# Kernel optimization log

Measured on AMD Instinct MI355X. Metric: run time of the kernel, lower is better.

## Reference

```python
import jax, jax.numpy as jnp
import numpy as np

D_IN = 1024
D_OUT = 1024
NUM_HEADS = 16
HEAD_DIM = D_OUT // NUM_HEADS


def setup_inputs() -> dict:
    key = jax.random.key(0)
    k_x, k_q, k_k, k_v, k_o = jax.random.split(key, 5)
    # Xavier-uniform-ish init for weights (stored as [d_in, d_out] for x @ W)
    lim = float(np.sqrt(6.0 / (D_IN + D_OUT)) / np.sqrt(2.0))
    lim_o = float(np.sqrt(6.0 / (D_OUT + D_OUT)))
    return {
        "x": jax.random.normal(k_x, (2, 2048, D_IN), dtype=jnp.float32),
        "W_query": jax.random.uniform(k_q, (D_IN, D_OUT), jnp.float32, -lim, lim),
        "W_key": jax.random.uniform(k_k, (D_IN, D_OUT), jnp.float32, -lim, lim),
        "W_value": jax.random.uniform(k_v, (D_IN, D_OUT), jnp.float32, -lim, lim),
        "W_out": jax.random.uniform(k_o, (D_OUT, D_OUT), jnp.float32, -lim_o, lim_o),
        "b_out": jnp.zeros((D_OUT,), dtype=jnp.float32),
    }


def reference(x, W_query, W_key, W_value, W_out, b_out):
    B, S, _ = x.shape
    scale = 1.0 / np.sqrt(HEAD_DIM)

    def split_heads(t):  # [B,S,D] -> [B,H,S,hd]
        return t.reshape(B, S, NUM_HEADS, HEAD_DIM).transpose(0, 2, 1, 3)

    q = split_heads(x @ W_query)
    k = split_heads(x @ W_key)
    v = split_heads(x @ W_value)

    scores = jnp.einsum("bhqd,bhkd->bhqk", q, k) * scale  # [B,H,S,S]
    causal = jnp.tril(jnp.ones((S, S), dtype=bool))  # True = keep
    scores = jnp.where(causal, scores, -jnp.inf)
    weights = jax.nn.softmax(scores, axis=-1)
    ctx = jnp.einsum("bhqk,bhkd->bhqd", weights, v)
    ctx = ctx.transpose(0, 2, 1, 3).reshape(B, S, D_OUT)
    return ctx @ W_out + b_out
```

## Files before the change

kernel.cpp:

```cpp
#include <hip/hip_runtime.h>
#include <hip/hip_bf16.h>


typedef __bf16 bf16_t;
typedef __bf16 bf16x4 __attribute__((ext_vector_type(4)));
typedef __bf16 bf16x8 __attribute__((ext_vector_type(8)));
typedef float f32x4 __attribute__((ext_vector_type(4)));

#define AS_GLOBAL __attribute__((address_space(1)))
#define AS_LDS    __attribute__((address_space(3)))

__device__ __forceinline__ void async_load16(const void* g, void* l) {
    __builtin_amdgcn_global_load_lds((AS_GLOBAL void*)(g), (AS_LDS void*)(l), 16, 0, 0);
}

__device__ __forceinline__ void barrier_lgkm() {
    asm volatile("s_waitcnt lgkmcnt(0)\n\ts_barrier" ::: "memory");
}

__global__ __launch_bounds__(256) void cvt_f32_bf16(const float* __restrict__ src,
                                                    bf16_t* __restrict__ dst, int n4) {
    int i = blockIdx.x * 256 + threadIdx.x;
    if (i < n4) {
        float4 v = ((const float4*)src)[i];
        bf16x4 o;
        o[0] = (bf16_t)v.x; o[1] = (bf16_t)v.y; o[2] = (bf16_t)v.z; o[3] = (bf16_t)v.w;
        ((bf16x4*)dst)[i] = o;
    }
}

__global__ __launch_bounds__(256) void transpose_cvt4(
    const float* __restrict__ W0, const float* __restrict__ W1,
    const float* __restrict__ W2, const float* __restrict__ W3,
    bf16_t* __restrict__ outbase) {
    __shared__ bf16_t T[64][65];
    int t = threadIdx.x;
    int k0 = blockIdx.x * 64, n0 = blockIdx.y * 64, z = blockIdx.z;
    const float* W = (z == 0) ? W0 : (z == 1) ? W1 : (z == 2) ? W2 : W3;
    bf16_t* WT = outbase + (size_t)z * 1048576;
#pragma unroll
    for (int c = 0; c < 4; c++) {
        int idx = c * 256 + t;
        int row = idx >> 4;
        int col4 = (idx & 15) * 4;
        float4 v = *(const float4*)(W + (k0 + row) * 1024 + n0 + col4);
        T[row][col4 + 0] = (bf16_t)v.x;
        T[row][col4 + 1] = (bf16_t)v.y;
        T[row][col4 + 2] = (bf16_t)v.z;
        T[row][col4 + 3] = (bf16_t)v.w;
    }
    __syncthreads();
#pragma unroll
    for (int c = 0; c < 4; c++) {
        int idx = c * 256 + t;
        int nrow = idx >> 4;
        int kc4 = (idx & 15) * 4;
        bf16x4 o;
        o[0] = T[kc4 + 0][nrow];
        o[1] = T[kc4 + 1][nrow];
        o[2] = T[kc4 + 2][nrow];
        o[3] = T[kc4 + 3][nrow];
        *(bf16x4*)(WT + (n0 + nrow) * 1024 + k0 + kc4) = o;
    }
}

__global__ __launch_bounds__(256) void qkv_gemm(
    const bf16_t* __restrict__ A,
    const bf16_t* __restrict__ WqT, const bf16_t* __restrict__ WkT,
    const bf16_t* __restrict__ WvT,
    bf16_t* __restrict__ Qo, bf16_t* __restrict__ Ko, bf16_t* __restrict__ Vo) {
    const int KD = 1024;
    __shared__ __align__(16) bf16_t As[2][4096];
    __shared__ __align__(16) bf16_t Bs[2][4096];
    int tid = threadIdx.x;
    int wave = tid >> 6, lane = tid & 63;
    int quad = lane >> 4, l16 = lane & 15;
    int wm = wave >> 1, wn = wave & 1;
    int z = blockIdx.z;
    const bf16_t* BT = (z == 0) ? WqT : (z == 1) ? WkT : WvT;
    int m0 = blockIdx.x * 128;
    int n0 = blockIdx.y * 128;

    int r = tid >> 2;
    int c8 = (((tid & 3) ^ ((tid >> 3) & 3))) * 8;
    const bf16_t* gA0 = A + (size_t)(m0 + r) * KD + c8;
    const bf16_t* gA1 = A + (size_t)(m0 + 64 + r) * KD + c8;
    const bf16_t* gB0 = BT + (size_t)(n0 + r) * KD + c8;
    const bf16_t* gB1 = BT + (size_t)(n0 + 64 + r) * KD + c8;

    f32x4 acc[4][4];
#pragma unroll
    for (int i = 0; i < 4; i++)
#pragma unroll
        for (int j = 0; j < 4; j++) acc[i][j] = (f32x4){0.f, 0.f, 0.f, 0.f};

    int4 sa0 = *(const int4*)gA0, sa1 = *(const int4*)gA1;
    int4 sb0 = *(const int4*)gB0, sb1 = *(const int4*)gB1;
    *(int4*)(As[0] + tid * 8) = sa0;
    *(int4*)(As[0] + 2048 + tid * 8) = sa1;
    *(int4*)(Bs[0] + tid * 8) = sb0;
    *(int4*)(Bs[0] + 2048 + tid * 8) = sb1;
    sa0 = *(const int4*)(gA0 + 32); sa1 = *(const int4*)(gA1 + 32);
    sb0 = *(const int4*)(gB0 + 32); sb1 = *(const int4*)(gB1 + 32);

    int csw = (quad ^ ((l16 >> 1) & 3)) * 8;
#pragma unroll 1
    for (int kk = 0; kk < 32; kk += 2) {
        barrier_lgkm();
        bf16x8 af[4], bfr[4];
#pragma unroll
        for (int mt = 0; mt < 4; mt++)
            af[mt] = *(const bf16x8*)(As[0] + (wm * 64 + mt * 16 + l16) * 32 + csw);
#pragma unroll
        for (int nt = 0; nt < 4; nt++)
            bfr[nt] = *(const bf16x8*)(Bs[0] + (wn * 64 + nt * 16 + l16) * 32 + csw);
        *(int4*)(As[1] + tid * 8) = sa0;
        *(int4*)(As[1] + 2048 + tid * 8) = sa1;
        *(int4*)(Bs[1] + tid * 8) = sb0;
        *(int4*)(Bs[1] + 2048 + tid * 8) = sb1;
        if (kk + 2 < 32) {
            int k0 = (kk + 2) * 32;
            sa0 = *(const int4*)(gA0 + k0); sa1 = *(const int4*)(gA1 + k0);
            sb0 = *(const int4*)(gB0 + k0); sb1 = *(const int4*)(gB1 + k0);
        }
        if (z == 2) {
#pragma unroll
            for (int mt = 0; mt < 4; mt++)
#pragma unroll
                for (int nt = 0; nt < 4; nt++)
                    acc[mt][nt] = __builtin_amdgcn_mfma_f32_16x16x32_bf16(
                        bfr[nt], af[mt], acc[mt][nt], 0, 0, 0);
        } else {
#pragma unroll
            for (int mt = 0; mt < 4; mt++)
#pragma unroll
                for (int nt = 0; nt < 4; nt++)
                    acc[mt][nt] = __builtin_amdgcn_mfma_f32_16x16x32_bf16(
                        af[mt], bfr[nt], acc[mt][nt], 0, 0, 0);
        }
        barrier_lgkm();
#pragma unroll
        for (int mt = 0; mt < 4; mt++)
            af[mt] = *(const bf16x8*)(As[1] + (wm * 64 + mt * 16 + l16) * 32 + csw);
#pragma unroll
        for (int nt = 0; nt < 4; nt++)
            bfr[nt] = *(const bf16x8*)(Bs[1] + (wn * 64 + nt * 16 + l16) * 32 + csw);
        if (kk + 2 < 32) {
            *(int4*)(As[0] + tid * 8) = sa0;
            *(int4*)(As[0] + 2048 + tid * 8) = sa1;
            *(int4*)(Bs[0] + tid * 8) = sb0;
            *(int4*)(Bs[0] + 2048 + tid * 8) = sb1;
            if (kk + 3 < 32) {
                int k0 = (kk + 3) * 32;
                sa0 = *(const int4*)(gA0 + k0); sa1 = *(const int4*)(gA1 + k0);
                sb0 = *(const int4*)(gB0 + k0); sb1 = *(const int4*)(gB1 + k0);
            }
        }
        if (z == 2) {
#pragma unroll
            for (int mt = 0; mt < 4; mt++)
#pragma unroll
                for (int nt = 0; nt < 4; nt++)
                    acc[mt][nt] = __builtin_amdgcn_mfma_f32_16x16x32_bf16(
                        bfr[nt], af[mt], acc[mt][nt], 0, 0, 0);
        } else {
#pragma unroll
            for (int mt = 0; mt < 4; mt++)
#pragma unroll
                for (int nt = 0; nt < 4; nt++)
                    acc[mt][nt] = __builtin_amdgcn_mfma_f32_16x16x32_bf16(
                        af[mt], bfr[nt], acc[mt][nt], 0, 0, 0);
        }
    }

    if (z == 0) {
#pragma unroll
        for (int mt = 0; mt < 4; mt++) {
            int mg_base = m0 + wm * 64 + mt * 16 + quad * 4;
#pragma unroll
            for (int nt = 0; nt < 4; nt++) {
                int ng = n0 + wn * 64 + nt * 16 + l16;
                int h = ng >> 6, d = ng & 63;
#pragma unroll
                for (int rr = 0; rr < 4; rr++) {
                    int mg = mg_base + rr;
                    int b = mg >> 11, s = mg & 2047;
                    Qo[(((size_t)(b * 16 + h) * 2048) + s) * 64 + d] =
                        (bf16_t)acc[mt][nt][rr];
                }
            }
        }
    } else if (z == 1) {
#pragma unroll
        for (int mt = 0; mt < 4; mt++) {
            int mg_base = m0 + wm * 64 + mt * 16 + quad * 4;
#pragma unroll
            for (int nt = 0; nt < 4; nt++) {
                int ng = n0 + wn * 64 + nt * 16 + l16;
                int h = ng >> 6, dd = ng & 63;
#pragma unroll
                for (int rr = 0; rr < 4; rr++) {
                    int mg = mg_base + rr;
                    int b = mg >> 11, sl = mg & 2047;
                    int kt = sl >> 6, row = sl & 63;
                    int cc = (dd >> 3) ^ (row & 7);
                    Ko[(size_t)(b * 16 + h) * 131072 + kt * 4096 + row * 64 +
                       cc * 8 + (dd & 7)] = (bf16_t)acc[mt][nt][rr];
                }
            }
        }
    } else {
#pragma unroll
        for (int mt = 0; mt < 4; mt++) {
            int sg = m0 + wm * 64 + mt * 16 + l16;
            int b = sg >> 11, sl = sg & 2047;
            int kt = sl >> 6, srow = sl & 63;
#pragma unroll
            for (int nt = 0; nt < 4; nt++) {
                int dg_base = n0 + wn * 64 + nt * 16 + quad * 4;
#pragma unroll
                for (int rr = 0; rr < 4; rr++) {
                    int dg = dg_base + rr;
                    int h = dg >> 6, dd = dg & 63;
                    int cc = (srow >> 3) ^ (dd & 7);
                    Vo[(size_t)(b * 16 + h) * 131072 + kt * 4096 + dd * 64 +
                       cc * 8 + (srow & 7)] = (bf16_t)acc[mt][nt][rr];
                }
            }
        }
    }
}

__device__ __forceinline__ float exp_pwrite(f32x4 sc[4], bf16_t* Ps,
                                            int wave, int quad, int l16) {
    float part = 0.f;
    int rowbase = (wave * 16 + l16) * 64;
    int gran = (quad & 1) * 4;
    int chi = quad >> 1;
#pragma unroll
    for (int nt = 0; nt < 4; nt++) {
        f32x4 p;
#pragma unroll
        for (int rr = 0; rr < 4; rr++) {
            p[rr] = __builtin_amdgcn_exp2f(sc[nt][rr]);
            part += p[rr];
        }
        bf16x4 pb;
#pragma unroll
        for (int rr = 0; rr < 4; rr++) pb[rr] = (bf16_t)p[rr];
        int cc = (nt * 2 + chi) ^ (l16 & 7);
        *(bf16x4*)(Ps + rowbase + cc * 8 + gran) = pb;
    }
    part += __shfl_xor(part, 16);
    part += __shfl_xor(part, 32);
    return part;
}

__global__ __launch_bounds__(256) void attn(
    const bf16_t* __restrict__ Q, const bf16_t* __restrict__ Kt,
    const bf16_t* __restrict__ Vt, bf16_t* __restrict__ ctx) {
    const int S = 2048;
    __shared__ bf16_t Ks[2][4096];
    __shared__ bf16_t Vs[2][4096];
    __shared__ bf16_t Ps[4096];
    int tid = threadIdx.x, wave = tid >> 6, lane = tid & 63;
    int quad = lane >> 4, l16 = lane & 15;

    int f = blockIdx.x + 32 * blockIdx.y;
    int g = f >> 8, s = f & 255;
    int qt = (g & 1) ? (31 - (s & 31)) : (s & 31);
    int bh = (s >> 5) + 8 * g;
    int h = bh & 15, b = bh >> 4;

    const bf16_t* Qbh = Q + (size_t)bh * S * 64;
    const bf16_t* Kbh = Kt + (size_t)bh * 131072;
    const bf16_t* Vbh = Vt + (size_t)bh * 131072;

    const float qs = 0.125f * 1.44269504f;
    bf16x8 aQ[2];
    {
        const bf16_t* rq = Qbh + (size_t)(qt * 64 + wave * 16 + l16) * 64;
#pragma unroll
        for (int ks = 0; ks < 2; ks++) {
            bf16x8 t = *(const bf16x8*)(rq + ks * 32 + quad * 8);
#pragma unroll
            for (int j = 0; j < 8; j++) t[j] = (bf16_t)((float)t[j] * qs);
            aQ[ks] = t;
        }
    }

    float L = 0.f;
    f32x4 O[4];
#pragma unroll
    for (int i = 0; i < 4; i++) O[i] = (f32x4){0.f, 0.f, 0.f, 0.f};

    {
        const bf16_t* kg = Kbh + tid * 8;
        const bf16_t* vg = Vbh + tid * 8;
        async_load16(kg, Ks[0] + wave * 512);
        async_load16(kg + 2048, Ks[0] + 2048 + wave * 512);
        async_load16(vg, Vs[0] + wave * 512);
        async_load16(vg + 2048, Vs[0] + 2048 + wave * 512);
    }
    __syncthreads();

    for (int kt = 0; kt <= qt; kt++) {
        int cur = kt & 1;
        if (kt < qt) {
            const bf16_t* kg = Kbh + (kt + 1) * 4096 + tid * 8;
            const bf16_t* vg = Vbh + (kt + 1) * 4096 + tid * 8;
            async_load16(kg, Ks[cur ^ 1] + wave * 512);
            async_load16(kg + 2048, Ks[cur ^ 1] + 2048 + wave * 512);
            async_load16(vg, Vs[cur ^ 1] + wave * 512);
            async_load16(vg + 2048, Vs[cur ^ 1] + 2048 + wave * 512);
        }

        bf16x8 kf[4][2], vf[4][2];
#pragma unroll
        for (int nt = 0; nt < 4; nt++) {
            const bf16_t* krow = Ks[cur] + (nt * 16 + l16) * 64;
            const bf16_t* vrow = Vs[cur] + (nt * 16 + l16) * 64;
#pragma unroll
            for (int ks = 0; ks < 2; ks++) {
                int csw = ((ks * 4 + quad) ^ (l16 & 7)) * 8;
                kf[nt][ks] = *(const bf16x8*)(krow + csw);
                vf[nt][ks] = *(const bf16x8*)(vrow + csw);
            }
        }

        f32x4 sc[4];
#pragma unroll
        for (int nt = 0; nt < 4; nt++) {
            f32x4 ss = (f32x4){0.f, 0.f, 0.f, 0.f};
            ss = __builtin_amdgcn_mfma_f32_16x16x32_bf16(kf[nt][0], aQ[0], ss, 0, 0, 0);
            ss = __builtin_amdgcn_mfma_f32_16x16x32_bf16(kf[nt][1], aQ[1], ss, 0, 0, 0);
            sc[nt] = ss;
        }
        if (kt == qt) {
            int qg = qt * 64 + wave * 16 + l16;
#pragma unroll
            for (int nt = 0; nt < 4; nt++)
#pragma unroll
                for (int rr = 0; rr < 4; rr++)
                    if (kt * 64 + nt * 16 + quad * 4 + rr > qg) sc[nt][rr] = -1e30f;
        }
        L += exp_pwrite(sc, Ps, wave, quad, l16);

#pragma unroll
        for (int ks = 0; ks < 2; ks++) {
            int csw = ((ks * 4 + quad) ^ (l16 & 7)) * 8;
            bf16x8 aP = *(const bf16x8*)(Ps + (wave * 16 + l16) * 64 + csw);
#pragma unroll
            for (int nt = 0; nt < 4; nt++)
                O[nt] = __builtin_amdgcn_mfma_f32_16x16x32_bf16(aP, vf[nt][ks],
                                                                O[nt], 0, 0, 0);
        }
        __syncthreads();
    }

    float il[4];
#pragma unroll
    for (int rr = 0; rr < 4; rr++) il[rr] = 1.f / __shfl(L, quad * 4 + rr);
#pragma unroll
    for (int nt = 0; nt < 4; nt++) {
#pragma unroll
        for (int rr = 0; rr < 4; rr++) {
            int qoff = wave * 16 + quad * 4 + rr;
            int col = h * 64 + nt * 16 + l16;
            ctx[(size_t)(b * 2048 + qt * 64 + qoff) * 1024 + col] =
                (bf16_t)(O[nt][rr] * il[rr]);
        }
    }
}

__global__ __launch_bounds__(256) void out_gemm(
    const bf16_t* __restrict__ A, const bf16_t* __restrict__ BT,
    const float* __restrict__ bias, float* __restrict__ Cout) {
    const int KD = 1024;
    __shared__ __align__(16) bf16_t As[2][2048];
    __shared__ __align__(16) bf16_t Bs[2][4096];
    int tid = threadIdx.x;
    int wave = tid >> 6, lane = tid & 63;
    int quad = lane >> 4, l16 = lane & 15;
    int wm = wave >> 1, wn = wave & 1;
    int m0 = blockIdx.x * 64;
    int n0 = blockIdx.y * 128;

    int r = tid >> 2;
    int c8 = (((tid & 3) ^ ((tid >> 3) & 3))) * 8;
    const bf16_t* gA  = A + (size_t)(m0 + r) * KD + c8;
    const bf16_t* gB0 = BT + (size_t)(n0 + r) * KD + c8;
    const bf16_t* gB1 = BT + (size_t)(n0 + 64 + r) * KD + c8;

    f32x4 acc[2][4];
#pragma unroll
    for (int i = 0; i < 2; i++)
#pragma unroll
        for (int j = 0; j < 4; j++) acc[i][j] = (f32x4){0.f, 0.f, 0.f, 0.f};

    int4 sa = *(const int4*)gA;
    int4 sb0 = *(const int4*)gB0, sb1 = *(const int4*)gB1;
    *(int4*)(As[0] + tid * 8) = sa;
    *(int4*)(Bs[0] + tid * 8) = sb0;
    *(int4*)(Bs[0] + 2048 + tid * 8) = sb1;
    sa = *(const int4*)(gA + 32);
    sb0 = *(const int4*)(gB0 + 32); sb1 = *(const int4*)(gB1 + 32);

    int csw = (quad ^ ((l16 >> 1) & 3)) * 8;
#pragma unroll 1
    for (int kk = 0; kk < 32; kk += 2) {
        barrier_lgkm();
        bf16x8 af[2], bfr[4];
#pragma unroll
        for (int mt = 0; mt < 2; mt++)
            af[mt] = *(const bf16x8*)(As[0] + (wm * 32 + mt * 16 + l16) * 32 + csw);
#pragma unroll
        for (int nt = 0; nt < 4; nt++)
            bfr[nt] = *(const bf16x8*)(Bs[0] + (wn * 64 + nt * 16 + l16) * 32 + csw);
        *(int4*)(As[1] + tid * 8) = sa;
        *(int4*)(Bs[1] + tid * 8) = sb0;
        *(int4*)(Bs[1] + 2048 + tid * 8) = sb1;
        if (kk + 2 < 32) {
            int k0 = (kk + 2) * 32;
            sa = *(const int4*)(gA + k0);
            sb0 = *(const int4*)(gB0 + k0); sb1 = *(const int4*)(gB1 + k0);
        }
#pragma unroll
        for (int mt = 0; mt < 2; mt++)
#pragma unroll
            for (int nt = 0; nt < 4; nt++)
                acc[mt][nt] = __builtin_amdgcn_mfma_f32_16x16x32_bf16(af[mt], bfr[nt],
                                                                      acc[mt][nt], 0, 0, 0);
        barrier_lgkm();
#pragma unroll
        for (int mt = 0; mt < 2; mt++)
            af[mt] = *(const bf16x8*)(As[1] + (wm * 32 + mt * 16 + l16) * 32 + csw);
#pragma unroll
        for (int nt = 0; nt < 4; nt++)
            bfr[nt] = *(const bf16x8*)(Bs[1] + (wn * 64 + nt * 16 + l16) * 32 + csw);
        if (kk + 2 < 32) {
            *(int4*)(As[0] + tid * 8) = sa;
            *(int4*)(Bs[0] + tid * 8) = sb0;
            *(int4*)(Bs[0] + 2048 + tid * 8) = sb1;
            if (kk + 3 < 32) {
                int k0 = (kk + 3) * 32;
                sa = *(const int4*)(gA + k0);
                sb0 = *(const int4*)(gB0 + k0); sb1 = *(const int4*)(gB1 + k0);
            }
        }
#pragma unroll
        for (int mt = 0; mt < 2; mt++)
#pragma unroll
            for (int nt = 0; nt < 4; nt++)
                acc[mt][nt] = __builtin_amdgcn_mfma_f32_16x16x32_bf16(af[mt], bfr[nt],
                                                                      acc[mt][nt], 0, 0, 0);
    }

#pragma unroll
    for (int mt = 0; mt < 2; mt++) {
        int mg_base = m0 + wm * 32 + mt * 16 + quad * 4;
#pragma unroll
        for (int nt = 0; nt < 4; nt++) {
            int ng = n0 + wn * 64 + nt * 16 + l16;
            float bv = bias[ng];
#pragma unroll
            for (int rr = 0; rr < 4; rr++) {
                int mg = mg_base + rr;
                Cout[(size_t)mg * 1024 + ng] = acc[mt][nt][rr] + bv;
            }
        }
    }
}

extern "C" void kernel_launch(void* const* d_in, const int* in_sizes, int n_in,
                              void* d_out, int out_size, void* d_ws, size_t ws_size,
                              hipStream_t stream) {
    const float* x  = (const float*)d_in[0];
    const float* Wq = (const float*)d_in[1];
    const float* Wk = (const float*)d_in[2];
    const float* Wv = (const float*)d_in[3];
    const float* Wo = (const float*)d_in[4];
    const float* bo = (const float*)d_in[5];
    float* out = (float*)d_out;
    char* ws = (char*)d_ws;

    bf16_t* xb   = (bf16_t*)(ws);
    bf16_t* WTs  = (bf16_t*)(ws + (8u << 20));
    bf16_t* WqT  = WTs;
    bf16_t* WkT  = WTs + 1048576;
    bf16_t* WvT  = WTs + 2097152;
    bf16_t* WoT  = WTs + 3145728;
    bf16_t* Qb   = (bf16_t*)(ws + (16u << 20));
    bf16_t* Kb   = (bf16_t*)(ws + (24u << 20));
    bf16_t* Vb   = (bf16_t*)(ws + (32u << 20));
    bf16_t* ctxb = (bf16_t*)(ws + (40u << 20));

    cvt_f32_bf16<<<4096, 256, 0, stream>>>(x, xb, (4096 * 1024) / 4);
    transpose_cvt4<<<dim3(16, 16, 4), 256, 0, stream>>>(Wq, Wk, Wv, Wo, WTs);
    qkv_gemm<<<dim3(32, 8, 3), 256, 0, stream>>>(xb, WqT, WkT, WvT, Qb, Kb, Vb);
    attn<<<dim3(32, 32), 256, 0, stream>>>(Qb, Kb, Vb, ctxb);
    out_gemm<<<dim3(64, 8), 256, 0, stream>>>(ctxb, WoT, bo, out);
}
```

Baseline: 186.6 us.

## Fuse x conversion into QKV GEMM and process two query tiles per attention block

Removes the separate f32-to-bf16 conversion kernel by loading fp32 x directly in the QKV GEMM and converting to bf16 as tiles are staged into LDS. The attention kernel now handles 128 query rows per block as two 64-row subtiles that share each loaded K/V tile, halving K/V traffic and block count. It also swaps the async global_load_lds path for register-staged prefetch two tiles ahead. Costs include doubled fp32 A-tile global reads in the GEMM, more registers per attention thread, and coarser causal load balance.

```diff
diff --git a/kernel.cpp b/kernel.cpp
--- a/kernel.cpp
+++ b/kernel.cpp
@@ -10,23 +10,15 @@
 #define AS_GLOBAL __attribute__((address_space(1)))
 #define AS_LDS    __attribute__((address_space(3)))
 
-__device__ __forceinline__ void async_load16(const void* g, void* l) {
-    __builtin_amdgcn_global_load_lds((AS_GLOBAL void*)(g), (AS_LDS void*)(l), 16, 0, 0);
-}
-
 __device__ __forceinline__ void barrier_lgkm() {
     asm volatile("s_waitcnt lgkmcnt(0)\n\ts_barrier" ::: "memory");
 }
 
-__global__ __launch_bounds__(256) void cvt_f32_bf16(const float* __restrict__ src,
-                                                    bf16_t* __restrict__ dst, int n4) {
-    int i = blockIdx.x * 256 + threadIdx.x;
-    if (i < n4) {
-        float4 v = ((const float4*)src)[i];
-        bf16x4 o;
-        o[0] = (bf16_t)v.x; o[1] = (bf16_t)v.y; o[2] = (bf16_t)v.z; o[3] = (bf16_t)v.w;
-        ((bf16x4*)dst)[i] = o;
-    }
+__device__ __forceinline__ bf16x8 cvt_bf8(float4 lo, float4 hi) {
+    bf16x8 r;
+    r[0] = (bf16_t)lo.x; r[1] = (bf16_t)lo.y; r[2] = (bf16_t)lo.z; r[3] = (bf16_t)lo.w;
+    r[4] = (bf16_t)hi.x; r[5] = (bf16_t)hi.y; r[6] = (bf16_t)hi.z; r[7] = (bf16_t)hi.w;
+    return r;
 }
 
 __global__ __launch_bounds__(256) void transpose_cvt4(
@@ -65,7 +57,7 @@
 }
 
 __global__ __launch_bounds__(256) void qkv_gemm(
-    const bf16_t* __restrict__ A,
+    const float* __restrict__ X,
     const bf16_t* __restrict__ WqT, const bf16_t* __restrict__ WkT,
     const bf16_t* __restrict__ WvT,
     bf16_t* __restrict__ Qo, bf16_t* __restrict__ Ko, bf16_t* __restrict__ Vo) {
@@ -83,8 +75,8 @@
 
     int r = tid >> 2;
     int c8 = (((tid & 3) ^ ((tid >> 3) & 3))) * 8;
-    const bf16_t* gA0 = A + (size_t)(m0 + r) * KD + c8;
-    const bf16_t* gA1 = A + (size_t)(m0 + 64 + r) * KD + c8;
+    const float*  gA0 = X + (size_t)(m0 + r) * KD + c8;
+    const float*  gA1 = X + (size_t)(m0 + 64 + r) * KD + c8;
     const bf16_t* gB0 = BT + (size_t)(n0 + r) * KD + c8;
     const bf16_t* gB1 = BT + (size_t)(n0 + 64 + r) * KD + c8;
 
@@ -94,13 +86,15 @@
 #pragma unroll
         for (int j = 0; j < 4; j++) acc[i][j] = (f32x4){0.f, 0.f, 0.f, 0.f};
 
-    int4 sa0 = *(const int4*)gA0, sa1 = *(const int4*)gA1;
+    float4 fa0l = *(const float4*)gA0, fa0h = *(const float4*)(gA0 + 4);
+    float4 fa1l = *(const float4*)gA1, fa1h = *(const float4*)(gA1 + 4);
     int4 sb0 = *(const int4*)gB0, sb1 = *(const int4*)gB1;
-    *(int4*)(As[0] + tid * 8) = sa0;
-    *(int4*)(As[0] + 2048 + tid * 8) = sa1;
+    *(bf16x8*)(As[0] + tid * 8) = cvt_bf8(fa0l, fa0h);
+    *(bf16x8*)(As[0] + 2048 + tid * 8) = cvt_bf8(fa1l, fa1h);
     *(int4*)(Bs[0] + tid * 8) = sb0;
     *(int4*)(Bs[0] + 2048 + tid * 8) = sb1;
-    sa0 = *(const int4*)(gA0 + 32); sa1 = *(const int4*)(gA1 + 32);
+    fa0l = *(const float4*)(gA0 + 32); fa0h = *(const float4*)(gA0 + 36);
+    fa1l = *(const float4*)(gA1 + 32); fa1h = *(const float4*)(gA1 + 36);
     sb0 = *(const int4*)(gB0 + 32); sb1 = *(const int4*)(gB1 + 32);
 
     int csw = (quad ^ ((l16 >> 1) & 3)) * 8;
@@ -114,13 +108,14 @@
 #pragma unroll
         for (int nt = 0; nt < 4; nt++)
             bfr[nt] = *(const bf16x8*)(Bs[0] + (wn * 64 + nt * 16 + l16) * 32 + csw);
-        *(int4*)(As[1] + tid * 8) = sa0;
-        *(int4*)(As[1] + 2048 + tid * 8) = sa1;
+        *(bf16x8*)(As[1] + tid * 8) = cvt_bf8(fa0l, fa0h);
+        *(bf16x8*)(As[1] + 2048 + tid * 8) = cvt_bf8(fa1l, fa1h);
         *(int4*)(Bs[1] + tid * 8) = sb0;
         *(int4*)(Bs[1] + 2048 + tid * 8) = sb1;
         if (kk + 2 < 32) {
             int k0 = (kk + 2) * 32;
-            sa0 = *(const int4*)(gA0 + k0); sa1 = *(const int4*)(gA1 + k0);
+            fa0l = *(const float4*)(gA0 + k0); fa0h = *(const float4*)(gA0 + k0 + 4);
+            fa1l = *(const float4*)(gA1 + k0); fa1h = *(const float4*)(gA1 + k0 + 4);
             sb0 = *(const int4*)(gB0 + k0); sb1 = *(const int4*)(gB1 + k0);
         }
         if (z == 2) {
@@ -146,13 +141,14 @@
         for (int nt = 0; nt < 4; nt++)
             bfr[nt] = *(const bf16x8*)(Bs[1] + (wn * 64 + nt * 16 + l16) * 32 + csw);
         if (kk + 2 < 32) {
-            *(int4*)(As[0] + tid * 8) = sa0;
-            *(int4*)(As[0] + 2048 + tid * 8) = sa1;
+            *(bf16x8*)(As[0] + tid * 8) = cvt_bf8(fa0l, fa0h);
+            *(bf16x8*)(As[0] + 2048 + tid * 8) = cvt_bf8(fa1l, fa1h);
             *(int4*)(Bs[0] + tid * 8) = sb0;
             *(int4*)(Bs[0] + 2048 + tid * 8) = sb1;
             if (kk + 3 < 32) {
                 int k0 = (kk + 3) * 32;
-                sa0 = *(const int4*)(gA0 + k0); sa1 = *(const int4*)(gA1 + k0);
+                fa0l = *(const float4*)(gA0 + k0); fa0h = *(const float4*)(gA0 + k0 + 4);
+                fa1l = *(const float4*)(gA1 + k0); fa1h = *(const float4*)(gA1 + k0 + 4);
                 sb0 = *(const int4*)(gB0 + k0); sb1 = *(const int4*)(gB1 + k0);
             }
         }
@@ -260,61 +256,60 @@
     const bf16_t* __restrict__ Q, const bf16_t* __restrict__ Kt,
     const bf16_t* __restrict__ Vt, bf16_t* __restrict__ ctx) {
     const int S = 2048;
-    __shared__ bf16_t Ks[2][4096];
-    __shared__ bf16_t Vs[2][4096];
-    __shared__ bf16_t Ps[4096];
+    __shared__ __align__(16) bf16_t Ks[2][4096];
+    __shared__ __align__(16) bf16_t Vs[2][4096];
+    __shared__ __align__(16) bf16_t Ps[2][4096];
     int tid = threadIdx.x, wave = tid >> 6, lane = tid & 63;
     int quad = lane >> 4, l16 = lane & 15;
 
     int f = blockIdx.x + 32 * blockIdx.y;
     int g = f >> 8, s = f & 255;
-    int qt = (g & 1) ? (31 - (s & 31)) : (s & 31);
-    int bh = (s >> 5) + 8 * g;
+    int qtj = g ? (15 - (s & 15)) : (s & 15);
+    int bh = (s >> 4) + 16 * g;
     int h = bh & 15, b = bh >> 4;
+    int q0 = qtj * 128;
 
     const bf16_t* Qbh = Q + (size_t)bh * S * 64;
     const bf16_t* Kbh = Kt + (size_t)bh * 131072;
     const bf16_t* Vbh = Vt + (size_t)bh * 131072;
 
     const float qs = 0.125f * 1.44269504f;
-    bf16x8 aQ[2];
-    {
-        const bf16_t* rq = Qbh + (size_t)(qt * 64 + wave * 16 + l16) * 64;
+    bf16x8 aQ[2][2];
+#pragma unroll
+    for (int sub = 0; sub < 2; sub++) {
+        const bf16_t* rq = Qbh + (size_t)(q0 + sub * 64 + wave * 16 + l16) * 64;
 #pragma unroll
         for (int ks = 0; ks < 2; ks++) {
             bf16x8 t = *(const bf16x8*)(rq + ks * 32 + quad * 8);
 #pragma unroll
             for (int j = 0; j < 8; j++) t[j] = (bf16_t)((float)t[j] * qs);
-            aQ[ks] = t;
-        }
-    }
-
-    float L = 0.f;
-    f32x4 O[4];
-#pragma unroll
-    for (int i = 0; i < 4; i++) O[i] = (f32x4){0.f, 0.f, 0.f, 0.f};
-
-    {
-        const bf16_t* kg = Kbh + tid * 8;
-        const bf16_t* vg = Vbh + tid * 8;
-        async_load16(kg, Ks[0] + wave * 512);
-        async_load16(kg + 2048, Ks[0] + 2048 + wave * 512);
-        async_load16(vg, Vs[0] + wave * 512);
-        async_load16(vg + 2048, Vs[0] + 2048 + wave * 512);
-    }
-    __syncthreads();
-
-    for (int kt = 0; kt <= qt; kt++) {
+            aQ[sub][ks] = t;
+        }
+    }
+
+    float L[2] = {0.f, 0.f};
+    f32x4 O[2][4];
+#pragma unroll
+    for (int sub = 0; sub < 2; sub++)
+#pragma unroll
+        for (int i = 0; i < 4; i++) O[sub][i] = (f32x4){0.f, 0.f, 0.f, 0.f};
+
+    int tmax = 2 * qtj + 2;
+    int4 ska = *(const int4*)(Kbh + tid * 8);
+    int4 skb = *(const int4*)(Kbh + 2048 + tid * 8);
+    int4 sva = *(const int4*)(Vbh + tid * 8);
+    int4 svb = *(const int4*)(Vbh + 2048 + tid * 8);
+    *(int4*)(Ks[0] + tid * 8) = ska; *(int4*)(Ks[0] + 2048 + tid * 8) = skb;
+    *(int4*)(Vs[0] + tid * 8) = sva; *(int4*)(Vs[0] + 2048 + tid * 8) = svb;
+    ska = *(const int4*)(Kbh + 4096 + tid * 8);
+    skb = *(const int4*)(Kbh + 6144 + tid * 8);
+    sva = *(const int4*)(Vbh + 4096 + tid * 8);
+    svb = *(const int4*)(Vbh + 6144 + tid * 8);
+
+#pragma unroll 1
+    for (int kt = 0; kt < tmax; kt++) {
         int cur = kt & 1;
-        if (kt < qt) {
-            const bf16_t* kg = Kbh + (kt + 1) * 4096 + tid * 8;
-            const bf16_t* vg = Vbh + (kt + 1) * 4096 + tid * 8;
-            async_load16(kg, Ks[cur ^ 1] + wave * 512);
-            async_load16(kg + 2048, Ks[cur ^ 1] + 2048 + wave * 512);
-            async_load16(vg, Vs[cur ^ 1] + wave * 512);
-            async_load16(vg + 2048, Vs[cur ^ 1] + 2048 + wave * 512);
-        }
-
+        barrier_lgkm();
         bf16x8 kf[4][2], vf[4][2];
 #pragma unroll
         for (int nt = 0; nt < 4; nt++) {
@@ -327,48 +322,92 @@
                 vf[nt][ks] = *(const bf16x8*)(vrow + csw);
             }
         }
-
-        f32x4 sc[4];
-#pragma unroll
-        for (int nt = 0; nt < 4; nt++) {
-            f32x4 ss = (f32x4){0.f, 0.f, 0.f, 0.f};
-            ss = __builtin_amdgcn_mfma_f32_16x16x32_bf16(kf[nt][0], aQ[0], ss, 0, 0, 0);
-            ss = __builtin_amdgcn_mfma_f32_16x16x32_bf16(kf[nt][1], aQ[1], ss, 0, 0, 0);
-            sc[nt] = ss;
-        }
-        if (kt == qt) {
-            int qg = qt * 64 + wave * 16 + l16;
-#pragma unroll
-            for (int nt = 0; nt < 4; nt++)
-#pragma unroll
-                for (int rr = 0; rr < 4; rr++)
-                    if (kt * 64 + nt * 16 + quad * 4 + rr > qg) sc[nt][rr] = -1e30f;
-        }
-        L += exp_pwrite(sc, Ps, wave, quad, l16);
+        if (kt + 1 < tmax) {
+            *(int4*)(Ks[cur ^ 1] + tid * 8) = ska;
+            *(int4*)(Ks[cur ^ 1] + 2048 + tid * 8) = skb;
+            *(int4*)(Vs[cur ^ 1] + tid * 8) = sva;
+            *(int4*)(Vs[cur ^ 1] + 2048 + tid * 8) = svb;
+        }
+        if (kt + 2 < tmax) {
+            const bf16_t* kg = Kbh + (kt + 2) * 4096;
+            const bf16_t* vg = Vbh + (kt + 2) * 4096;
+            ska = *(const int4*)(kg + tid * 8);
+            skb = *(const int4*)(kg + 2048 + tid * 8);
+            sva = *(const int4*)(vg + tid * 8);
+            svb = *(const int4*)(vg + 2048 + tid * 8);
+        }
+
+        bool do_lo = (kt < tmax - 1);
+        if (do_lo) {
+            f32x4 sc[4];
+#pragma unroll
+            for (int nt = 0; nt < 4; nt++) {
+                f32x4 ss = (f32x4){0.f, 0.f, 0.f, 0.f};
+                ss = __builtin_amdgcn_mfma_f32_16x16x32_bf16(kf[nt][0], aQ[0][0], ss, 0, 0, 0);
+                ss = __builtin_amdgcn_mfma_f32_16x16x32_bf16(kf[nt][1], aQ[0][1], ss, 0, 0, 0);
+                sc[nt] = ss;
+            }
+            if (kt == tmax - 2) {
+                int qg = q0 + wave * 16 + l16;
+#pragma unroll
+                for (int nt = 0; nt < 4; nt++)
+#pragma unroll
+                    for (int rr = 0; rr < 4; rr++)
+                        if (kt * 64 + nt * 16 + quad * 4 + rr > qg) sc[nt][rr] = -1e30f;
+            }
+            L[0] += exp_pwrite(sc, Ps[0], wave, quad, l16);
+        }
+        {
+            f32x4 sc[4];
+#pragma unroll
+            for (int nt = 0; nt < 4; nt++) {
+                f32x4 ss = (f32x4){0.f, 0.f, 0.f, 0.f};
+                ss = __builtin_amdgcn_mfma_f32_16x16x32_bf16(kf[nt][0], aQ[1][0], ss, 0, 0, 0);
+                ss = __builtin_amdgcn_mfma_f32_16x16x32_bf16(kf[nt][1], aQ[1][1], ss, 0, 0, 0);
+                sc[nt] = ss;
+            }
+            if (kt == tmax - 1) {
+                int qg = q0 + 64 + wave * 16 + l16;
+#pragma unroll
+                for (int nt = 0; nt < 4; nt++)
+#pragma unroll
+                    for (int rr = 0; rr < 4; rr++)
+                        if (kt * 64 + nt * 16 + quad * 4 + rr > qg) sc[nt][rr] = -1e30f;
+            }
+            L[1] += exp_pwrite(sc, Ps[1], wave, quad, l16);
+        }
 
 #pragma unroll
         for (int ks = 0; ks < 2; ks++) {
             int csw = ((ks * 4 + quad) ^ (l16 & 7)) * 8;
-            bf16x8 aP = *(const bf16x8*)(Ps + (wave * 16 + l16) * 64 + csw);
-#pragma unroll
-            for (int nt = 0; nt < 4; nt++)
-                O[nt] = __builtin_amdgcn_mfma_f32_16x16x32_bf16(aP, vf[nt][ks],
-                                                                O[nt], 0, 0, 0);
-        }
-        __syncthreads();
-    }
-
-    float il[4];
-#pragma unroll
-    for (int rr = 0; rr < 4; rr++) il[rr] = 1.f / __shfl(L, quad * 4 + rr);
-#pragma unroll
-    for (int nt = 0; nt < 4; nt++) {
-#pragma unroll
-        for (int rr = 0; rr < 4; rr++) {
-            int qoff = wave * 16 + quad * 4 + rr;
-            int col = h * 64 + nt * 16 + l16;
-            ctx[(size_t)(b * 2048 + qt * 64 + qoff) * 1024 + col] =
-                (bf16_t)(O[nt][rr] * il[rr]);
+            bf16x8 aPhi = *(const bf16x8*)(Ps[1] + (wave * 16 + l16) * 64 + csw);
+            bf16x8 aPlo;
+            if (do_lo) aPlo = *(const bf16x8*)(Ps[0] + (wave * 16 + l16) * 64 + csw);
+#pragma unroll
+            for (int nt = 0; nt < 4; nt++) {
+                O[1][nt] = __builtin_amdgcn_mfma_f32_16x16x32_bf16(aPhi, vf[nt][ks],
+                                                                   O[1][nt], 0, 0, 0);
+                if (do_lo)
+                    O[0][nt] = __builtin_amdgcn_mfma_f32_16x16x32_bf16(aPlo, vf[nt][ks],
+                                                                       O[0][nt], 0, 0, 0);
+            }
+        }
+    }
+
+#pragma unroll
+    for (int sub = 0; sub < 2; sub++) {
+        float il[4];
+#pragma unroll
+        for (int rr = 0; rr < 4; rr++) il[rr] = 1.f / __shfl(L[sub], quad * 4 + rr);
+#pragma unroll
+        for (int nt = 0; nt < 4; nt++) {
+#pragma unroll
+            for (int rr = 0; rr < 4; rr++) {
+                int qoff = q0 + sub * 64 + wave * 16 + quad * 4 + rr;
+                int col = h * 64 + nt * 16 + l16;
+                ctx[(size_t)(b * 2048 + qoff) * 1024 + col] =
+                    (bf16_t)(O[sub][nt][rr] * il[rr]);
+            }
         }
     }
 }
@@ -484,7 +523,6 @@
     float* out = (float*)d_out;
     char* ws = (char*)d_ws;
 
-    bf16_t* xb   = (bf16_t*)(ws);
     bf16_t* WTs  = (bf16_t*)(ws + (8u << 20));
     bf16_t* WqT  = WTs;
     bf16_t* WkT  = WTs + 1048576;
@@ -495,9 +533,8 @@
     bf16_t* Vb   = (bf16_t*)(ws + (32u << 20));
     bf16_t* ctxb = (bf16_t*)(ws + (40u << 20));
 
-    cvt_f32_bf16<<<4096, 256, 0, stream>>>(x, xb, (4096 * 1024) / 4);
     transpose_cvt4<<<dim3(16, 16, 4), 256, 0, stream>>>(Wq, Wk, Wv, Wo, WTs);
-    qkv_gemm<<<dim3(32, 8, 3), 256, 0, stream>>>(xb, WqT, WkT, WvT, Qb, Kb, Vb);
-    attn<<<dim3(32, 32), 256, 0, stream>>>(Qb, Kb, Vb, ctxb);
+    qkv_gemm<<<dim3(32, 8, 3), 256, 0, stream>>>(x, WqT, WkT, WvT, Qb, Kb, Vb);
+    attn<<<dim3(32, 16), 256, 0, stream>>>(Qb, Kb, Vb, ctxb);
     out_gemm<<<dim3(64, 8), 256, 0, stream>>>(ctxb, WoT, bo, out);
 }
```

Result: no change. 186.9 us (+0.2%).
